# Kernel optimization log

Hardware: AMD Instinct MI355X
Metric: run time of the kernel (lower is better)

## Reference

```python
import jax, jax.numpy as jnp
import numpy as np

N_NODES = 50000
N_EDGES = 800000
D_IN = 128
D_OUT = 128


def setup_inputs() -> dict:
    key = jax.random.key(0)
    k1, k2, k3, k4, k5 = jax.random.split(key, 5)
    x = jax.random.normal(k1, (N_NODES, D_IN), dtype=jnp.float32)
    edge_index = jax.random.randint(k2, (2, N_EDGES), 0, N_NODES, dtype=jnp.int64)
    # PyG SAGEConv params: lin_l (neighbors, with bias), lin_r (root, no bias)
    scale = 1.0 / np.sqrt(D_IN)
    W_l = jax.random.uniform(k3, (D_OUT, D_IN), dtype=jnp.float32, minval=-scale, maxval=scale)
    b_l = jax.random.uniform(k4, (D_OUT,), dtype=jnp.float32, minval=-scale, maxval=scale)
    W_r = jax.random.uniform(k5, (D_OUT, D_IN), dtype=jnp.float32, minval=-scale, maxval=scale)
    return {"x": x, "edge_index": edge_index, "W_l": W_l, "b_l": b_l, "W_r": W_r}


def reference(x, edge_index, W_l, b_l, W_r):
    src, dst = edge_index[0], edge_index[1]
    # mean aggregation of neighbor (source) features into destination nodes
    msg = x[src]  # [E, D_IN]
    agg_sum = jax.ops.segment_sum(msg, dst, num_segments=N_NODES)  # [N, D_IN]
    deg = jax.ops.segment_sum(jnp.ones((N_EDGES,), dtype=x.dtype), dst, num_segments=N_NODES)
    agg = agg_sum / jnp.maximum(deg, 1.0)[:, None]  # isolated nodes -> 0
    # out = lin_l(agg) + lin_r(x); ReLU from SAGE_NET wrapper (active=True)
    out = agg @ W_l.T + b_l + x @ W_r.T
    return jax.nn.relu(out)
```

## Files before the change

### kernel.cpp

```cpp
#include <hip/hip_runtime.h>
#include <hip/hip_bf16.h>

#define NNODES 50000
#define NEDGES 800000
#define DD 128
#define CAP 64
#define NSCAN 256
#define SLICE 782
#define NT4 (NEDGES / 4)
#define NBKT 256
#define BKTW 196
#define XCV_B 6250
#define WPK_B 64
#define WKB3 (NSCAN + XCV_B + WPK_B)
#define WP2 68
#define ZROW ((u32)NNODES)

typedef unsigned int u32;
typedef unsigned short u16;
typedef short bf16x8 __attribute__((ext_vector_type(8)));
typedef float f32x4 __attribute__((ext_vector_type(4)));
typedef float f32x2 __attribute__((ext_vector_type(2)));

#if defined(__has_builtin)
#if __has_builtin(__builtin_amdgcn_cvt_pk_f32_fp8)
#define HAVE_HW_FP8 1
#endif
#endif

union U4B8 {
    uint4 u;
    bf16x8 b;
};

__device__ __forceinline__ u32 f2b(float f) {
    u32 u = __float_as_uint(f);
    u32 rounding = 0x7fffu + ((u >> 16) & 1u);
    return (u + rounding) >> 16;
}

__device__ __forceinline__ u32 f2e4m3(float f) {
    u32 u = __float_as_uint(f);
    u32 s = (u >> 31) << 7;
    u32 mag = u & 0x7fffffffu;
    if (mag < 0x3c800000u) return s;
    u32 t = mag + 0x0007FFFFu + ((mag >> 20) & 1u);
    u32 e = (t >> 23) - 120u;
    u32 m = (t >> 20) & 7u;
    if (e > 15u || (e == 15u && m == 7u)) { e = 15u; m = 6u; }
    return s | (e << 3) | m;
}

__device__ __forceinline__ void fp8x4_acc(u32 v, float& a0, float& a1,
                                          float& a2, float& a3) {
#ifdef HAVE_HW_FP8
    f32x2 lo = __builtin_amdgcn_cvt_pk_f32_fp8((int)v, false);
    f32x2 hi = __builtin_amdgcn_cvt_pk_f32_fp8((int)v, true);
    a0 += lo.x;
    a1 += lo.y;
    a2 += hi.x;
    a3 += hi.y;
#else
#pragma unroll
    for (int b = 0; b < 4; ++b) {
        u32 byte = (v >> (8 * b)) & 0xffu;
        u32 f = ((byte >> 7) << 31) | ((((byte >> 3) & 15u) + 120u) << 23) |
                ((byte & 7u) << 20);
        float val = (byte & 0x78u) ? __uint_as_float(f) : 0.f;
        if (b == 0) a0 += val;
        else if (b == 1) a1 += val;
        else if (b == 2) a2 += val;
        else a3 += val;
    }
#endif
}

__global__ __launch_bounds__(256) void work_k(
    const int* __restrict__ ei, u32* __restrict__ totals,
    u32* __restrict__ claim, const float* __restrict__ x,
    u32* __restrict__ xb, u32* __restrict__ xq,
    const float* __restrict__ Wl, const float* __restrict__ Wr,
    u32* __restrict__ wb) {
    __shared__ u32 hist[NBKT];
    const int b = blockIdx.x, tid = threadIdx.x;
    if (b < NSCAN) {
        const u32 s = (u32)b;
        if (tid < NBKT) hist[tid] = 0u;
        __syncthreads();
        const u32 T0 = s * SLICE;
        const u32 T1 = min(T0 + (u32)SLICE, (u32)NT4);
        for (u32 t4 = T0 + tid; t4 < T1; t4 += 256u) {
            uint4 dv = ((const uint4*)(ei + NEDGES))[t4];
            atomicAdd(&hist[dv.x / BKTW], 1u);
            atomicAdd(&hist[dv.y / BKTW], 1u);
            atomicAdd(&hist[dv.z / BKTW], 1u);
            atomicAdd(&hist[dv.w / BKTW], 1u);
        }
        __syncthreads();
        if (tid < NBKT) {
            u32 c = hist[tid];
            claim[s * NBKT + tid] = c ? atomicAdd(&totals[tid], c) : 0u;
        }
    } else if (b < NSCAN + XCV_B) {
        int i = (b - NSCAN) * 256 + tid;
        float4 v = ((const float4*)x)[i];
        uint2 o;
        o.x = f2b(v.x) | (f2b(v.y) << 16);
        o.y = f2b(v.z) | (f2b(v.w) << 16);
        ((uint2*)xb)[i] = o;
        xq[i] = f2e4m3(v.x) | (f2e4m3(v.y) << 8) | (f2e4m3(v.z) << 16) |
                (f2e4m3(v.w) << 24);
    } else {
        int idx = (b - NSCAN - XCV_B) * 256 + tid;
        int o = idx >> 7, c = idx & 127, k0 = 2 * c;
        const float* src = (k0 < DD) ? (Wl + o * DD + k0) : (Wr + o * DD + (k0 - DD));
        wb[idx] = f2b(src[0]) | (f2b(src[1]) << 16);
        if (b == WKB3 - 1 && tid < 32)
            xq[(size_t)ZROW * 32 + tid] = 0u;
    }
}

__global__ __launch_bounds__(256) void place_k(
    const int* __restrict__ ei, const u32* __restrict__ totals,
    const u32* __restrict__ claim, u32* __restrict__ sorted) {
    __shared__ u32 tot[NBKT], base[NBKT], lcnt[NBKT];
    const u32 s = blockIdx.x;
    const int tid = threadIdx.x;
    if (tid < NBKT) {
        tot[tid] = totals[tid];
        lcnt[tid] = 0u;
    }
    __syncthreads();
    if (tid == 0) {
        u32 acc = 0;
        for (int i = 0; i < NBKT; ++i) { base[i] = acc; acc += tot[i]; }
    }
    __syncthreads();
    const u32 T0 = s * SLICE;
    const u32 T1 = min(T0 + (u32)SLICE, (u32)NT4);
    for (u32 t4 = T0 + tid; t4 < T1; t4 += 256u) {
        uint4 dv = ((const uint4*)(ei + NEDGES))[t4];
        uint4 sv = ((const uint4*)ei)[t4];
#pragma unroll
        for (int k = 0; k < 4; ++k) {
            u32 d = k == 0 ? dv.x : k == 1 ? dv.y : k == 2 ? dv.z : dv.w;
            u32 sr = k == 0 ? sv.x : k == 1 ? sv.y : k == 2 ? sv.z : sv.w;
            u32 bk = d / BKTW;
            u32 loc = atomicAdd(&lcnt[bk], 1u);
            sorted[base[bk] + claim[s * NBKT + bk] + loc] = (sr << 16) | d;
        }
    }
}

__global__ __launch_bounds__(256) void fill2_k(
    const u32* __restrict__ sorted, const u32* __restrict__ totals,
    u32* __restrict__ deg, u16* __restrict__ slots16) {
    __shared__ u32 cnt[BKTW];
    __shared__ u32 sbase, stot;
    const u32 g = blockIdx.x;
    const int tid = threadIdx.x;
    if (tid < BKTW) cnt[tid] = 0u;
    if (tid == 0) {
        u32 acc = 0;
        for (u32 i = 0; i < g; ++i) acc += totals[i];
        sbase = acc;
        stot = totals[g];
    }
    __syncthreads();
    const u32 E0 = sbase, E1 = sbase + stot;
    const u32 nbase = g * BKTW;
    for (u32 idx = E0 + tid; idx < E1; idx += 256u) {
        u32 e = sorted[idx];
        u32 d = e & 0xffffu;
        u32 sr = e >> 16;
        u32 pos = atomicAdd(&cnt[d - nbase], 1u);
        if (pos < CAP) slots16[(size_t)d * CAP + pos] = (u16)sr;
    }
    __syncthreads();
    for (u32 i = tid; i < (u32)BKTW; i += 256u) {
        u32 node = nbase + i;
        if (node < (u32)NNODES) deg[node] = cnt[i];
    }
}

__global__ __launch_bounds__(256) void gather_k(
    const u32* __restrict__ xq, const u16* __restrict__ slots16,
    const u32* __restrict__ deg, u32* __restrict__ aggb) {
    u32 gid = blockIdx.x * 256u + threadIdx.x;
    u32 node = gid >> 6;
    u32 lane = gid & 63u;
    if (node >= NNODES) return;
    u32 d = deg[node];
    u32 cnt = min(d, (u32)CAP);
    u32 svp = (lane < cnt) ? (u32)slots16[(size_t)node * CAP + lane] : ZROW;
    const u32 half = lane >> 5;
    const u32 q = lane & 31u;
    float a0 = 0.f, a1 = 0.f, a2 = 0.f, a3 = 0.f;
    for (u32 j = 0; j < cnt; j += 16) {
        u32 v[8];
#pragma unroll
        for (int p = 0; p < 8; ++p) {
            u32 sA = __shfl(svp, (int)(j + 2 * p), 64);
            u32 sB = __shfl(svp, (int)(j + 2 * p + 1), 64);
            u32 s = half ? sB : sA;
            v[p] = xq[(size_t)s * 32 + q];
        }
#pragma unroll
        for (int p = 0; p < 8; ++p) fp8x4_acc(v[p], a0, a1, a2, a3);
    }
    a0 += __shfl_xor(a0, 32, 64);
    a1 += __shfl_xor(a1, 32, 64);
    a2 += __shfl_xor(a2, 32, 64);
    a3 += __shfl_xor(a3, 32, 64);
    if (lane < 32) {
        float inv = 1.0f / fmaxf((float)d, 1.0f);
        uint2 o;
        o.x = f2b(a0 * inv) | (f2b(a1 * inv) << 16);
        o.y = f2b(a2 * inv) | (f2b(a3 * inv) << 16);
        *(uint2*)&aggb[(size_t)node * 64 + q * 2] = o;
    }
}

__global__ __launch_bounds__(512, 4) void gemm_k(
    const u32* __restrict__ aggb, const u32* __restrict__ xb,
    const u32* __restrict__ wb, const float* __restrict__ bl,
    float* __restrict__ out) {
    __shared__ u32 w2[DD * WP2];
    __shared__ float sbias[DD];
    const int tid = threadIdx.x;
    const int row0 = blockIdx.x * 64;
    const int wave = tid >> 6, lane = tid & 63;
    const int m = lane & 15, quad = lane >> 4;
    const int rw = wave & 3;
    const int ch = wave >> 2;

    uint4 af_a[4], af_x[4];
    {
        int r = row0 + rw * 16 + m;
        r = r < NNODES ? r : NNODES - 1;
        const u32* arow = aggb + (size_t)r * 64;
        const u32* xrow = xb + (size_t)r * 64;
#pragma unroll
        for (int ks = 0; ks < 4; ++ks) {
            af_a[ks] = *(const uint4*)&arow[ks * 16 + quad * 4];
            af_x[ks] = *(const uint4*)&xrow[ks * 16 + quad * 4];
        }
    }

    for (int r = tid >> 5; r < DD; r += 16) {
        int c2 = (tid & 31) * 2;
        *(uint2*)&w2[r * WP2 + c2] = *(const uint2*)&wb[r * DD + c2];
    }
    if (tid < DD) sbias[tid] = bl[tid];
    __syncthreads();

    f32x4 acc[4];
#pragma unroll
    for (int nt = 0; nt < 4; ++nt) acc[nt] = (f32x4){0.f, 0.f, 0.f, 0.f};

#pragma unroll
    for (int ks = 0; ks < 4; ++ks) {
        U4B8 af;
        af.u = af_a[ks];
#pragma unroll
        for (int nt = 0; nt < 4; ++nt) {
            U4B8 bf;
            bf.u = *(const uint4*)&w2[((ch * 4 + nt) * 16 + m) * WP2 + ks * 16 +
                                      quad * 4];
            acc[nt] = __builtin_amdgcn_mfma_f32_16x16x32_bf16(af.b, bf.b,
                                                              acc[nt], 0, 0, 0);
        }
    }
    __syncthreads();
    for (int r = tid >> 5; r < DD; r += 16) {
        int c2 = (tid & 31) * 2;
        *(uint2*)&w2[r * WP2 + c2] = *(const uint2*)&wb[r * DD + 64 + c2];
    }
    __syncthreads();

#pragma unroll
    for (int ks = 0; ks < 4; ++ks) {
        U4B8 af;
        af.u = af_x[ks];
#pragma unroll
        for (int nt = 0; nt < 4; ++nt) {
            U4B8 bf;
            bf.u = *(const uint4*)&w2[((ch * 4 + nt) * 16 + m) * WP2 + ks * 16 +
                                      quad * 4];
            acc[nt] = __builtin_amdgcn_mfma_f32_16x16x32_bf16(af.b, bf.b,
                                                              acc[nt], 0, 0, 0);
        }
    }

#pragma unroll
    for (int nt = 0; nt < 4; ++nt) {
        int col = (ch * 4 + nt) * 16 + m;
        float b = sbias[col];
#pragma unroll
        for (int r_ = 0; r_ < 4; ++r_) {
            int row = row0 + rw * 16 + quad * 4 + r_;
            if (row < NNODES)
                out[(size_t)row * DD + col] = fmaxf(acc[nt][r_] + b, 0.f);
        }
    }
}

__global__ __launch_bounds__(256) void scatter_k(
    const float* __restrict__ x, const int* __restrict__ ei,
    float* __restrict__ agg, u32* __restrict__ deg) {
    u32 gid = blockIdx.x * 256u + threadIdx.x;
    u32 edge = gid >> 6;
    u32 lane = gid & 63u;
    if (edge >= NEDGES) return;
    int src = ei[edge];
    int dst = ei[NEDGES + edge];
    float2 v = ((const float2*)(x + (size_t)src * DD))[lane];
    float* p = agg + (size_t)dst * DD + lane * 2u;
    unsafeAtomicAdd(p, v.x);
    unsafeAtomicAdd(p + 1, v.y);
    if (lane == 0) atomicAdd(deg + dst, 1u);
}

__global__ __launch_bounds__(256) void mean_k(
    float* __restrict__ agg, const u32* __restrict__ deg) {
    u32 gid = blockIdx.x * 256u + threadIdx.x;
    u32 node = gid >> 6;
    u32 lane = gid & 63u;
    if (node >= NNODES) return;
    float inv = 1.0f / fmaxf((float)deg[node], 1.0f);
    float2* p = (float2*)(agg + (size_t)node * DD) + lane;
    float2 v = *p;
    *p = make_float2(v.x * inv, v.y * inv);
}

__global__ __launch_bounds__(256) void lin_l_k(
    float* __restrict__ agg,
    const float* __restrict__ Wl, const float* __restrict__ bl) {
    __shared__ u32 WT[DD * 65];
    __shared__ float rows[4 * DD];
    __shared__ float sbias[DD];
    const int tid = threadIdx.x;
    {
        u16* WTs = (u16*)WT;
        for (int i = tid; i < DD * DD; i += 256) {
            int o = i >> 7, k = i & 127;
            WTs[k * 130 + o] = (u16)f2b(Wl[i]);
        }
        if (tid < DD) sbias[tid] = bl[tid];
    }
    __syncthreads();
    const int h = tid & 63;
    const int nl = tid >> 6;
    for (int base = blockIdx.x * 4; base < NNODES; base += gridDim.x * 4) {
        ((float2*)rows)[tid] =
            ((const float2*)(agg + (size_t)(base + (tid >> 6)) * DD))[tid & 63];
        __syncthreads();
        float acc0 = sbias[2 * h], acc1 = sbias[2 * h + 1];
#pragma unroll
        for (int k = 0; k < DD; ++k) {
            float a = rows[nl * DD + k];
            u32 w2 = WT[k * 65 + h];
            acc0 = fmaf(a, __uint_as_float(w2 << 16), acc0);
            acc1 = fmaf(a, __uint_as_float(w2 & 0xffff0000u), acc1);
        }
        __syncthreads();
        ((float2*)(agg + (size_t)(base + nl) * DD))[h] = make_float2(acc0, acc1);
    }
}

__global__ __launch_bounds__(256) void lin_r_k(
    float* __restrict__ io, const float* __restrict__ x,
    const float* __restrict__ Wr) {
    __shared__ u32 WT[DD * 65];
    __shared__ float rows[4 * DD];
    const int tid = threadIdx.x;
    {
        u16* WTs = (u16*)WT;
        for (int i = tid; i < DD * DD; i += 256) {
            int o = i >> 7, k = i & 127;
            WTs[k * 130 + o] = (u16)f2b(Wr[i]);
        }
    }
    __syncthreads();
    const int h = tid & 63;
    const int nl = tid >> 6;
    for (int base = blockIdx.x * 4; base < NNODES; base += gridDim.x * 4) {
        ((float2*)rows)[tid] =
            ((const float2*)(x + (size_t)(base + (tid >> 6)) * DD))[tid & 63];
        __syncthreads();
        float2 t2 = ((const float2*)(io + (size_t)(base + nl) * DD))[h];
        float acc0 = t2.x, acc1 = t2.y;
#pragma unroll
        for (int k = 0; k < DD; ++k) {
            float a = rows[nl * DD + k];
            u32 w2 = WT[k * 65 + h];
            acc0 = fmaf(a, __uint_as_float(w2 << 16), acc0);
            acc1 = fmaf(a, __uint_as_float(w2 & 0xffff0000u), acc1);
        }
        acc0 = fmaxf(acc0, 0.f);
        acc1 = fmaxf(acc1, 0.f);
        __syncthreads();
        ((float2*)(io + (size_t)(base + nl) * DD))[h] = make_float2(acc0, acc1);
    }
}

extern "C" void kernel_launch(void* const* d_in, const int* in_sizes, int n_in,
                              void* d_out, int out_size, void* d_ws, size_t ws_size,
                              hipStream_t stream) {
    const float* x  = (const float*)d_in[0];
    const int*   ei = (const int*)d_in[1];
    const float* Wl = (const float*)d_in[2];
    const float* bl = (const float*)d_in[3];
    const float* Wr = (const float*)d_in[4];

    u32* totals  = (u32*)d_ws;
    u32* claim   = totals + NBKT;
    u32* sorted  = claim + (size_t)NSCAN * NBKT;
    u32* deg     = sorted + NEDGES;
    u16* slots16 = (u16*)(deg + NNODES);
    u32* wb      = deg + NNODES + (size_t)NNODES * (CAP / 2);
    u32* xb      = wb + 16384;
    u32* xq      = xb + (size_t)NNODES * 64;
    u32* aggb    = xq + (size_t)NNODES * 32 + 32;
    const size_t need =
        ((size_t)NBKT + (size_t)NSCAN * NBKT + NEDGES +
         (size_t)NNODES * (1 + CAP / 2 + 64 + 32 + 64) + 16384 + 32) * 4;

    if (ws_size >= need) {
        hipMemsetAsync(totals, 0, NBKT * sizeof(u32), stream);
        work_k<<<WKB3, 256, 0, stream>>>(
            ei, totals, claim, x, xb, xq, Wl, Wr, wb);
        place_k<<<NSCAN, 256, 0, stream>>>(ei, totals, claim, sorted);
        fill2_k<<<NBKT, 256, 0, stream>>>(sorted, totals, deg, slots16);
        gather_k<<<12500, 256, 0, stream>>>(xq, slots16, deg, aggb);
        gemm_k<<<(NNODES + 63) / 64, 512, 0, stream>>>(
            aggb, xb, wb, bl, (float*)d_out);
    } else {
        float* agg = (float*)d_out;
        hipMemsetAsync(d_out, 0, (size_t)NNODES * DD * sizeof(float), stream);
        hipMemsetAsync(d_ws, 0, (size_t)NNODES * sizeof(u32), stream);
        scatter_k<<<(NEDGES * 64) / 256, 256, 0, stream>>>(x, ei, agg, deg);
        mean_k<<<(NNODES * 64 + 255) / 256, 256, 0, stream>>>(agg, deg);
        lin_l_k<<<1024, 256, 0, stream>>>(agg, Wl, bl);
        lin_r_k<<<1024, 256, 0, stream>>>(agg, x, Wr);
    }
}
```

Baseline: 151.0 us.

## Drop global totals atomics and spread x conversion across sort kernels

Scan blocks now write their per-bucket histograms directly instead of atomically claiming offsets in a global totals array. Later kernels derive each bucket's totals and prefix offsets by summing the claim matrix. This removes the memset and the global atomics. The x-to-bf16/fp8 conversion is split into three parts that run as extra blocks in work_k, place_k and fill2_k, overlapping with the sort phases. In exchange, every place/fill block now redundantly reads the whole 256x256 claim matrix.

Result: slower. 155.8 us (+3.2%).

```diff
diff --git a/kernel.cpp b/kernel.cpp
--- a/kernel.cpp
+++ b/kernel.cpp
@@ -10,9 +10,9 @@
 #define NT4 (NEDGES / 4)
 #define NBKT 256
 #define BKTW 196
-#define XCV_B 6250
+#define XSPLIT 2084
+#define XCV_TOT 6250
 #define WPK_B 64
-#define WKB3 (NSCAN + XCV_B + WPK_B)
 #define WP2 68
 #define ZROW ((u32)NNODES)
 
@@ -75,17 +75,28 @@
 #endif
 }
 
+__device__ __forceinline__ void xconv_body(const float* __restrict__ x,
+                                           u32* __restrict__ xb,
+                                           u32* __restrict__ xq, int i) {
+    float4 v = ((const float4*)x)[i];
+    uint2 o;
+    o.x = f2b(v.x) | (f2b(v.y) << 16);
+    o.y = f2b(v.z) | (f2b(v.w) << 16);
+    ((uint2*)xb)[i] = o;
+    xq[i] = f2e4m3(v.x) | (f2e4m3(v.y) << 8) | (f2e4m3(v.z) << 16) |
+            (f2e4m3(v.w) << 24);
+}
+
 __global__ __launch_bounds__(256) void work_k(
-    const int* __restrict__ ei, u32* __restrict__ totals,
-    u32* __restrict__ claim, const float* __restrict__ x,
-    u32* __restrict__ xb, u32* __restrict__ xq,
+    const int* __restrict__ ei, u32* __restrict__ claim,
+    const float* __restrict__ x, u32* __restrict__ xb, u32* __restrict__ xq,
     const float* __restrict__ Wl, const float* __restrict__ Wr,
     u32* __restrict__ wb) {
     __shared__ u32 hist[NBKT];
     const int b = blockIdx.x, tid = threadIdx.x;
     if (b < NSCAN) {
         const u32 s = (u32)b;
-        if (tid < NBKT) hist[tid] = 0u;
+        hist[tid] = 0u;
         __syncthreads();
         const u32 T0 = s * SLICE;
         const u32 T1 = min(T0 + (u32)SLICE, (u32)NT4);
@@ -97,89 +108,102 @@
             atomicAdd(&hist[dv.w / BKTW], 1u);
         }
         __syncthreads();
-        if (tid < NBKT) {
-            u32 c = hist[tid];
-            claim[s * NBKT + tid] = c ? atomicAdd(&totals[tid], c) : 0u;
-        }
-    } else if (b < NSCAN + XCV_B) {
-        int i = (b - NSCAN) * 256 + tid;
-        float4 v = ((const float4*)x)[i];
-        uint2 o;
-        o.x = f2b(v.x) | (f2b(v.y) << 16);
-        o.y = f2b(v.z) | (f2b(v.w) << 16);
-        ((uint2*)xb)[i] = o;
-        xq[i] = f2e4m3(v.x) | (f2e4m3(v.y) << 8) | (f2e4m3(v.z) << 16) |
-                (f2e4m3(v.w) << 24);
+        claim[s * NBKT + tid] = hist[tid];
+    } else if (b < NSCAN + XSPLIT) {
+        u32 xi = (u32)(b - NSCAN);
+        if (xi < (u32)XCV_TOT) xconv_body(x, xb, xq, (int)xi * 256 + tid);
     } else {
-        int idx = (b - NSCAN - XCV_B) * 256 + tid;
+        int idx = (b - NSCAN - XSPLIT) * 256 + tid;
         int o = idx >> 7, c = idx & 127, k0 = 2 * c;
         const float* src = (k0 < DD) ? (Wl + o * DD + k0) : (Wr + o * DD + (k0 - DD));
         wb[idx] = f2b(src[0]) | (f2b(src[1]) << 16);
-        if (b == WKB3 - 1 && tid < 32)
+        if (b == NSCAN + XSPLIT + WPK_B - 1 && tid < 32)
             xq[(size_t)ZROW * 32 + tid] = 0u;
     }
 }
 
 __global__ __launch_bounds__(256) void place_k(
-    const int* __restrict__ ei, const u32* __restrict__ totals,
-    const u32* __restrict__ claim, u32* __restrict__ sorted) {
-    __shared__ u32 tot[NBKT], base[NBKT], lcnt[NBKT];
-    const u32 s = blockIdx.x;
-    const int tid = threadIdx.x;
-    if (tid < NBKT) {
-        tot[tid] = totals[tid];
+    const int* __restrict__ ei, const u32* __restrict__ claim,
+    u32* __restrict__ sorted, const float* __restrict__ x,
+    u32* __restrict__ xb, u32* __restrict__ xq) {
+    __shared__ u32 precl[NBKT], base[NBKT], lcnt[NBKT], totsh[NBKT];
+    const int b = blockIdx.x, tid = threadIdx.x;
+    if (b < NSCAN) {
+        const u32 s = (u32)b;
+        u32 tot = 0, pre = 0;
+        for (int sp = 0; sp < NSCAN; ++sp) {
+            u32 c = claim[(u32)sp * NBKT + tid];
+            tot += c;
+            if ((u32)sp < s) pre += c;
+        }
+        totsh[tid] = tot;
+        precl[tid] = pre;
         lcnt[tid] = 0u;
-    }
-    __syncthreads();
-    if (tid == 0) {
-        u32 acc = 0;
-        for (int i = 0; i < NBKT; ++i) { base[i] = acc; acc += tot[i]; }
-    }
-    __syncthreads();
-    const u32 T0 = s * SLICE;
-    const u32 T1 = min(T0 + (u32)SLICE, (u32)NT4);
-    for (u32 t4 = T0 + tid; t4 < T1; t4 += 256u) {
-        uint4 dv = ((const uint4*)(ei + NEDGES))[t4];
-        uint4 sv = ((const uint4*)ei)[t4];
-#pragma unroll
-        for (int k = 0; k < 4; ++k) {
-            u32 d = k == 0 ? dv.x : k == 1 ? dv.y : k == 2 ? dv.z : dv.w;
-            u32 sr = k == 0 ? sv.x : k == 1 ? sv.y : k == 2 ? sv.z : sv.w;
-            u32 bk = d / BKTW;
-            u32 loc = atomicAdd(&lcnt[bk], 1u);
-            sorted[base[bk] + claim[s * NBKT + bk] + loc] = (sr << 16) | d;
-        }
+        __syncthreads();
+        if (tid == 0) {
+            u32 acc = 0;
+            for (int i = 0; i < NBKT; ++i) { base[i] = acc; acc += totsh[i]; }
+        }
+        __syncthreads();
+        const u32 T0 = s * SLICE;
+        const u32 T1 = min(T0 + (u32)SLICE, (u32)NT4);
+        for (u32 t4 = T0 + tid; t4 < T1; t4 += 256u) {
+            uint4 dv = ((const uint4*)(ei + NEDGES))[t4];
+            uint4 sv = ((const uint4*)ei)[t4];
+#pragma unroll
+            for (int k = 0; k < 4; ++k) {
+                u32 d = k == 0 ? dv.x : k == 1 ? dv.y : k == 2 ? dv.z : dv.w;
+                u32 sr = k == 0 ? sv.x : k == 1 ? sv.y : k == 2 ? sv.z : sv.w;
+                u32 bk = d / BKTW;
+                u32 loc = atomicAdd(&lcnt[bk], 1u);
+                sorted[base[bk] + precl[bk] + loc] = (sr << 16) | d;
+            }
+        }
+    } else {
+        u32 xi = (u32)XSPLIT + (u32)(b - NSCAN);
+        if (xi < (u32)XCV_TOT) xconv_body(x, xb, xq, (int)xi * 256 + tid);
     }
 }
 
 __global__ __launch_bounds__(256) void fill2_k(
-    const u32* __restrict__ sorted, const u32* __restrict__ totals,
-    u32* __restrict__ deg, u16* __restrict__ slots16) {
+    const u32* __restrict__ sorted, const u32* __restrict__ claim,
+    u32* __restrict__ deg, u16* __restrict__ slots16,
+    const float* __restrict__ x, u32* __restrict__ xb, u32* __restrict__ xq) {
     __shared__ u32 cnt[BKTW];
-    __shared__ u32 sbase, stot;
-    const u32 g = blockIdx.x;
-    const int tid = threadIdx.x;
-    if (tid < BKTW) cnt[tid] = 0u;
-    if (tid == 0) {
-        u32 acc = 0;
-        for (u32 i = 0; i < g; ++i) acc += totals[i];
-        sbase = acc;
-        stot = totals[g];
-    }
-    __syncthreads();
-    const u32 E0 = sbase, E1 = sbase + stot;
-    const u32 nbase = g * BKTW;
-    for (u32 idx = E0 + tid; idx < E1; idx += 256u) {
-        u32 e = sorted[idx];
-        u32 d = e & 0xffffu;
-        u32 sr = e >> 16;
-        u32 pos = atomicAdd(&cnt[d - nbase], 1u);
-        if (pos < CAP) slots16[(size_t)d * CAP + pos] = (u16)sr;
-    }
-    __syncthreads();
-    for (u32 i = tid; i < (u32)BKTW; i += 256u) {
-        u32 node = nbase + i;
-        if (node < (u32)NNODES) deg[node] = cnt[i];
+    __shared__ u32 totsh[NBKT];
+    __shared__ u32 sbase_s, stot_s;
+    const int b = blockIdx.x, tid = threadIdx.x;
+    if (b < NBKT) {
+        const u32 g = (u32)b;
+        u32 tot = 0;
+        for (int sp = 0; sp < NSCAN; ++sp) tot += claim[(u32)sp * NBKT + tid];
+        totsh[tid] = tot;
+        if (tid < BKTW) cnt[tid] = 0u;
+        __syncthreads();
+        if (tid == 0) {
+            u32 acc = 0;
+            for (u32 i = 0; i < g; ++i) acc += totsh[i];
+            sbase_s = acc;
+            stot_s = totsh[g];
+        }
+        __syncthreads();
+        const u32 E0 = sbase_s, E1 = sbase_s + stot_s;
+        const u32 nbase = g * BKTW;
+        for (u32 idx = E0 + tid; idx < E1; idx += 256u) {
+            u32 e = sorted[idx];
+            u32 d = e & 0xffffu;
+            u32 sr = e >> 16;
+            u32 pos = atomicAdd(&cnt[d - nbase], 1u);
+            if (pos < CAP) slots16[(size_t)d * CAP + pos] = (u16)sr;
+        }
+        __syncthreads();
+        for (u32 i = tid; i < (u32)BKTW; i += 256u) {
+            u32 node = nbase + i;
+            if (node < (u32)NNODES) deg[node] = cnt[i];
+        }
+    } else {
+        u32 xi = 2u * (u32)XSPLIT + (u32)(b - NBKT);
+        if (xi < (u32)XCV_TOT) xconv_body(x, xb, xq, (int)xi * 256 + tid);
     }
 }
 
@@ -413,8 +437,7 @@
     const float* bl = (const float*)d_in[3];
     const float* Wr = (const float*)d_in[4];
 
-    u32* totals  = (u32*)d_ws;
-    u32* claim   = totals + NBKT;
+    u32* claim   = (u32*)d_ws;
     u32* sorted  = claim + (size_t)NSCAN * NBKT;
     u32* deg     = sorted + NEDGES;
     u16* slots16 = (u16*)(deg + NNODES);
@@ -423,24 +446,26 @@
     u32* xq      = xb + (size_t)NNODES * 64;
     u32* aggb    = xq + (size_t)NNODES * 32 + 32;
     const size_t need =
-        ((size_t)NBKT + (size_t)NSCAN * NBKT + NEDGES +
+        ((size_t)NSCAN * NBKT + NEDGES +
          (size_t)NNODES * (1 + CAP / 2 + 64 + 32 + 64) + 16384 + 32) * 4;
 
     if (ws_size >= need) {
-        hipMemsetAsync(totals, 0, NBKT * sizeof(u32), stream);
-        work_k<<<WKB3, 256, 0, stream>>>(
-            ei, totals, claim, x, xb, xq, Wl, Wr, wb);
-        place_k<<<NSCAN, 256, 0, stream>>>(ei, totals, claim, sorted);
-        fill2_k<<<NBKT, 256, 0, stream>>>(sorted, totals, deg, slots16);
+        work_k<<<NSCAN + XSPLIT + WPK_B, 256, 0, stream>>>(
+            ei, claim, x, xb, xq, Wl, Wr, wb);
+        place_k<<<NSCAN + XSPLIT, 256, 0, stream>>>(
+            ei, claim, sorted, x, xb, xq);
+        fill2_k<<<NBKT + XSPLIT, 256, 0, stream>>>(
+            sorted, claim, deg, slots16, x, xb, xq);
         gather_k<<<12500, 256, 0, stream>>>(xq, slots16, deg, aggb);
         gemm_k<<<(NNODES + 63) / 64, 512, 0, stream>>>(
             aggb, xb, wb, bl, (float*)d_out);
     } else {
         float* agg = (float*)d_out;
+        u32* fdeg = (u32*)d_ws;
         hipMemsetAsync(d_out, 0, (size_t)NNODES * DD * sizeof(float), stream);
         hipMemsetAsync(d_ws, 0, (size_t)NNODES * sizeof(u32), stream);
-        scatter_k<<<(NEDGES * 64) / 256, 256, 0, stream>>>(x, ei, agg, deg);
-        mean_k<<<(NNODES * 64 + 255) / 256, 256, 0, stream>>>(agg, deg);
+        scatter_k<<<(NEDGES * 64) / 256, 256, 0, stream>>>(x, ei, agg, fdeg);
+        mean_k<<<(NNODES * 64 + 255) / 256, 256, 0, stream>>>(agg, fdeg);
         lin_l_k<<<1024, 256, 0, stream>>>(agg, Wl, bl);
         lin_r_k<<<1024, 256, 0, stream>>>(agg, x, Wr);
     }
```
